# Performance work log

Hardware: AMD Instinct MI355X
Metric: run time of the kernel (lower is better)

Reference implementation:

```python
import jax, jax.numpy as jnp
import numpy as np

B, T, D, H = 1, 2048, 1024, 16
Dh = D // H
GSA_SCALE = 0.25
LN_EPS = 1e-5


def setup_inputs() -> dict:
    key = jax.random.key(0)
    ks = jax.random.split(key, 24)
    s = 0.02
    def W(k, din, dout):
        return jax.random.normal(k, (din, dout), jnp.float32) * s
    inp = dict(
        x=jax.random.normal(ks[0], (B, T, D), jnp.float32),
        mask=jnp.ones((B, T, T), jnp.bool_),
        # MultiHeadAttention params (linears[0..3] = q,k,v,o)
        mha_wq=W(ks[1], D, D), mha_bq=jnp.zeros((D,), jnp.float32),
        mha_wk=W(ks[2], D, D), mha_bk=jnp.zeros((D,), jnp.float32),
        mha_wv=W(ks[3], D, D), mha_bv=jnp.zeros((D,), jnp.float32),
        mha_wo=W(ks[4], D, D), mha_bo=jnp.zeros((D,), jnp.float32),
        # _GeodesicSelfAttention params
        gsa_wq=W(ks[5], D, D), gsa_bq=jnp.zeros((D,), jnp.float32),
        gsa_wk=W(ks[6], D, D), gsa_bk=jnp.zeros((D,), jnp.float32),
        gsa_wv=W(ks[7], D, D), gsa_bv=jnp.zeros((D,), jnp.float32),
        gsa_wo=W(ks[8], D, D), gsa_bo=jnp.zeros((D,), jnp.float32),
        log_diag=jnp.zeros((H, Dh), jnp.float32),  # nn.Parameter(torch.zeros(h, dk))
        # LayerNorms
        ln_mha_g=jnp.ones((D,), jnp.float32), ln_mha_b=jnp.zeros((D,), jnp.float32),
        ln_gsa_g=jnp.ones((D,), jnp.float32), ln_gsa_b=jnp.zeros((D,), jnp.float32),
        # mix scalar (initialized to -2.0 in __init__)
        gsa_mix=jnp.asarray(-2.0, jnp.float32),
        # gate: Linear(D,D) -> GELU -> Linear(D,1), last bias filled with 0.5
        gate_w1=W(ks[9], D, D), gate_b1=jnp.zeros((D,), jnp.float32),
        gate_w2=W(ks[10], D, 1), gate_b2=jnp.full((1,), 0.5, jnp.float32),
    )
    return inp


def _ln(x, g, b):
    m = x.mean(-1, keepdims=True)
    v = ((x - m) ** 2).mean(-1, keepdims=True)
    return (x - m) / jnp.sqrt(v + LN_EPS) * g + b


def _heads(y):  # [B,T,D] -> [B,H,T,Dh]
    return y.reshape(B, T, H, Dh).transpose(0, 2, 1, 3)


def _merge(y):  # [B,H,T,Dh] -> [B,T,D]
    return y.transpose(0, 2, 1, 3).reshape(B, T, D)


def _forward(x, mask, mha_wq, mha_bq, mha_wk, mha_bk, mha_wv, mha_bv, mha_wo, mha_bo,
             gsa_wq, gsa_bq, gsa_wk, gsa_bk, gsa_wv, gsa_bv, gsa_wo, gsa_bo,
             log_diag, ln_mha_g, ln_mha_b, ln_gsa_g, ln_gsa_b, gsa_mix,
             gate_w1, gate_b1, gate_w2, gate_b2):
    inv_sqrt_dh = 1.0 / jnp.sqrt(jnp.float32(Dh))
    m4 = mask[:, None, :, :]  # [B,1,T,T]

    # ---- standard MHA branch ----
    q = _heads(x @ mha_wq + mha_bq)
    k = _heads(x @ mha_wk + mha_bk)
    v = _heads(x @ mha_wv + mha_bv)
    scores = jnp.einsum('bhtd,bhsd->bhts', q, k) * inv_sqrt_dh
    scores = jnp.where(m4, scores, -jnp.inf)
    p = jax.nn.softmax(scores, axis=-1)
    mha_out = _merge(jnp.einsum('bhts,bhsd->bhtd', p, v)) @ mha_wo + mha_bo

    # ---- geodesic (Mahalanobis) branch ----
    qg = _heads(x @ gsa_wq + gsa_bq)
    kg = _heads(x @ gsa_wk + gsa_bk)
    vg = _heads(x @ gsa_wv + gsa_bv)
    diag = jax.nn.softplus(log_diag) + 1e-6          # [H,Dh]
    diag4 = diag[None, :, None, :]
    qM = qg * diag4
    q2M = (qg * qM).sum(-1)                           # [B,H,T]
    k2M = (kg * (kg * diag4)).sum(-1)                 # [B,H,T]
    cross = jnp.einsum('bhtd,bhsd->bhts', qM, kg)     # [B,H,T,T]
    dist = q2M[..., :, None] + k2M[..., None, :] - 2.0 * cross
    s = -0.5 * dist * inv_sqrt_dh
    s = jnp.where(m4, s, -jnp.inf)
    all_inf = jnp.all(jnp.isneginf(s), axis=-1, keepdims=True)
    s = jnp.where(all_inf, 0.0, s)
    pg = jax.nn.softmax(s * GSA_SCALE, axis=-1)
    gsa_out = _merge(jnp.einsum('bhts,bhsd->bhtd', pg, vg)) @ gsa_wo + gsa_bo

    # ---- gated mix ----
    mha_out = _ln(mha_out, ln_mha_g, ln_mha_b)
    gsa_out = jax.nn.sigmoid(gsa_mix) * _ln(gsa_out, ln_gsa_g, ln_gsa_b)
    g = jax.nn.gelu(x @ gate_w1 + gate_b1, approximate=False) @ gate_w2 + gate_b2
    alpha = 0.9 * jax.nn.sigmoid(g)                   # alpha_cap = 0.9, [B,T,1]
    return alpha * mha_out + (1.0 - alpha) * gsa_out


def reference(x, mask, mha_wq, mha_bq, mha_wk, mha_bk, mha_wv, mha_bv, mha_wo, mha_bo,
              gsa_wq, gsa_bq, gsa_wk, gsa_bk, gsa_wv, gsa_bv, gsa_wo, gsa_bo,
              log_diag, ln_mha_g, ln_mha_b, ln_gsa_g, ln_gsa_b, gsa_mix,
              gate_w1, gate_b1, gate_w2, gate_b2):
    return _forward(x, mask, mha_wq, mha_bq, mha_wk, mha_bk, mha_wv, mha_bv, mha_wo, mha_bo,
                    gsa_wq, gsa_bq, gsa_wk, gsa_bk, gsa_wv, gsa_bv, gsa_wo, gsa_bo,
                    log_diag, ln_mha_g, ln_mha_b, ln_gsa_g, ln_gsa_b, gsa_mix,
                    gate_w1, gate_b1, gate_w2, gate_b2)
```

## Files before the change

### kernel.cpp

```cpp
#include <hip/hip_runtime.h>
#include <stdint.h>

typedef unsigned short u16;
typedef u16   u16x4  __attribute__((ext_vector_type(4)));
typedef u16   u16x8  __attribute__((ext_vector_type(8)));
typedef __bf16 bf16x8 __attribute__((ext_vector_type(8)));
typedef float f32x4  __attribute__((ext_vector_type(4)));

#define SEQ   2048
#define DM    1024
#define NHEAD 16
#define DHEAD 64

#define QM_SCALE 0.180336880f
#define QG_SCALE 0.045084220f
#define K2_SCALE 0.022542110f

static __device__ __forceinline__ u16 f2b(float f) {
  uint32_t u = __float_as_uint(f);
  u += 0x7fffu + ((u >> 16) & 1u);
  return (u16)(u >> 16);
}
static __device__ __forceinline__ float b2f(u16 u) {
  return __uint_as_float(((uint32_t)u) << 16);
}

static __device__ __forceinline__ void gload16(const u16* g, u16* l) {
  __builtin_amdgcn_global_load_lds(
      (const __attribute__((address_space(1))) unsigned int*)g,
      (__attribute__((address_space(3))) unsigned int*)l, 16, 0, 0);
}

struct PrepArgs { const float* w[9]; u16* o[9];
                  const float* x; u16* xb; const float* log_diag; float* diag; };

__global__ __launch_bounds__(256) void prep_kernel(PrepArgs a) {
  const int z = blockIdx.z, tid = threadIdx.x;
  if (z == 9) {
    int b = blockIdx.y * 16 + blockIdx.x;
#pragma unroll
    for (int j = 0; j < 8; ++j) {
      int idx = b * 8192 + j * 1024 + tid * 4;
      float4 v = *(const float4*)&a.x[idx];
      u16x4 w = {f2b(v.x), f2b(v.y), f2b(v.z), f2b(v.w)};
      *(u16x4*)&a.xb[idx] = w;
    }
    if (b == 0) {
#pragma unroll
      for (int j = 0; j < 4; ++j) {
        int i = j * 256 + tid;
        float v = a.log_diag[i];
        float sp = (v > 20.f) ? v : log1pf(__expf(v));
        a.diag[i] = sp + 1e-6f;
      }
    }
    return;
  }
  const float* __restrict__ src = a.w[z];
  u16* __restrict__ dst = a.o[z];
  int r0 = blockIdx.y * 64, c0 = blockIdx.x * 64;
  __shared__ float tile[64][65];
  int r = tid >> 2, o8 = (tid & 3) * 16;
#pragma unroll
  for (int i = 0; i < 16; i += 4) {
    float4 v = *(const float4*)&src[(r0 + r) * DM + c0 + o8 + i];
    tile[r][o8 + i + 0] = v.x; tile[r][o8 + i + 1] = v.y;
    tile[r][o8 + i + 2] = v.z; tile[r][o8 + i + 3] = v.w;
  }
  __syncthreads();
  u16x8 w0, w1;
#pragma unroll
  for (int i = 0; i < 8; ++i) w0[i] = f2b(tile[o8 + i][r]);
#pragma unroll
  for (int i = 0; i < 8; ++i) w1[i] = f2b(tile[o8 + 8 + i][r]);
  *(u16x8*)&dst[(c0 + r) * DM + r0 + o8]     = w0;
  *(u16x8*)&dst[(c0 + r) * DM + r0 + o8 + 8] = w1;
}

struct GemmDesc { const u16* A; const u16* Bt; const float* bias; void* out;
                  float* aux; int mode; int k0; int klen; float scale; };
struct GemmParams { GemmDesc d[8]; const float* diag; };

#define MFMA16 __builtin_amdgcn_mfma_f32_16x16x32_bf16

__global__
__attribute__((amdgpu_flat_work_group_size(512, 512)))
__attribute__((amdgpu_waves_per_eu(2, 2)))
void gemm_bt_kernel(GemmParams p) {
  GemmDesc g = p.d[blockIdx.z];
  const int K = DM;
  const int m0 = blockIdx.y * 256, n0 = blockIdx.x * 256;
  const int tid = threadIdx.x;
  const int wave = tid >> 6, lane = tid & 63, ln = lane & 15, quad = lane >> 4;
  const int wm = wave >> 2, wn = wave & 3;

  __shared__ __align__(16) u16 As[2][256 * 64];
  __shared__ __align__(16) u16 Bs[2][256 * 64];

  const f32x4 fz = {0.f, 0.f, 0.f, 0.f};
  f32x4 c00=fz,c01=fz,c02=fz,c03=fz, c10=fz,c11=fz,c12=fz,c13=fz;
  f32x4 c20=fz,c21=fz,c22=fz,c23=fz, c30=fz,c31=fz,c32=fz,c33=fz;
  f32x4 c40=fz,c41=fz,c42=fz,c43=fz, c50=fz,c51=fz,c52=fz,c53=fz;
  f32x4 c60=fz,c61=fz,c62=fz,c63=fz, c70=fz,c71=fz,c72=fz,c73=fz;

  const int trow  = tid >> 3;
  const int dslot = (tid & 7) ^ (trow & 7);
  const u16* Ap = g.A  + (size_t)(m0 + trow) * K + g.k0 + dslot * 8;
  const u16* Bp = g.Bt + (size_t)(n0 + trow) * K + g.k0 + dslot * 8;

  const int swA = (quad ^ (ln & 7)) * 8;
  const int swB = ((4 + quad) ^ (ln & 7)) * 8;
  const int bA = (wm * 128 + ln) * 64;
  const int bB = (wn * 64 + ln) * 64;

#pragma unroll
  for (int s = 0; s < 4; ++s)
    gload16(Ap + (size_t)s * 64 * K, &As[0][s * 4096 + tid * 8]);
#pragma unroll
  for (int s = 0; s < 4; ++s)
    gload16(Bp + (size_t)s * 64 * K, &Bs[0][s * 4096 + tid * 8]);

#define MB_STEP(SW, MB, A0, A1, A2, A3) {                                   \
    bf16x8 af = *(const bf16x8*)&As[cur][bA + (MB)*1024 + (SW)];            \
    A0 = MFMA16(af, b0, A0, 0, 0, 0); A1 = MFMA16(af, b1, A1, 0, 0, 0);     \
    A2 = MFMA16(af, b2, A2, 0, 0, 0); A3 = MFMA16(af, b3, A3, 0, 0, 0); }

#define KH_STEP(SW) {                                                       \
    bf16x8 b0 = *(const bf16x8*)&Bs[cur][bB +    0 + (SW)];                 \
    bf16x8 b1 = *(const bf16x8*)&Bs[cur][bB + 1024 + (SW)];                 \
    bf16x8 b2 = *(const bf16x8*)&Bs[cur][bB + 2048 + (SW)];                 \
    bf16x8 b3 = *(const bf16x8*)&Bs[cur][bB + 3072 + (SW)];                 \
    MB_STEP(SW, 0, c00, c01, c02, c03)  MB_STEP(SW, 1, c10, c11, c12, c13)  \
    MB_STEP(SW, 2, c20, c21, c22, c23)  MB_STEP(SW, 3, c30, c31, c32, c33)  \
    MB_STEP(SW, 4, c40, c41, c42, c43)  MB_STEP(SW, 5, c50, c51, c52, c53)  \
    MB_STEP(SW, 6, c60, c61, c62, c63)  MB_STEP(SW, 7, c70, c71, c72, c73) }

  const int nt = g.klen >> 6;
  int cur = 0;
  for (int t = 0; t < nt; ++t) {
    if (t + 1 < nt) {
      const int kk = (t + 1) << 6;
#pragma unroll
      for (int s = 0; s < 4; ++s)
        gload16(Ap + (size_t)s * 64 * K + kk, &As[cur ^ 1][s * 4096 + tid * 8]);
#pragma unroll
      for (int s = 0; s < 4; ++s)
        gload16(Bp + (size_t)s * 64 * K + kk, &Bs[cur ^ 1][s * 4096 + tid * 8]);
      asm volatile("s_waitcnt vmcnt(8)\n\ts_barrier" ::: "memory");
    } else {
      asm volatile("s_waitcnt vmcnt(0)\n\ts_barrier" ::: "memory");
    }
    KH_STEP(swA)
    KH_STEP(swB)
    asm volatile("s_barrier" ::: "memory");
    cur ^= 1;
  }

  const int mode = g.mode;

#define EPI_ONE(NB, A) {                                                    \
    const int col = n0 + wn * 64 + (NB) * 16 + ln;                          \
    const float bv = g.bias ? g.bias[col] : 0.f;                            \
    if (mode == 5) {                                                        \
      u16x4 w;                                                              \
      _Pragma("unroll") for (int r = 0; r < 4; ++r) w[r] = f2b(A[r] + bv);  \
      *(u16x4*)&((u16*)g.out)[(size_t)col * SEQ + row] = w;                 \
    } else {                                                                \
      _Pragma("unroll") for (int r = 0; r < 4; ++r) {                       \
        float v = A[r] + bv; int rw = row + r;                              \
        if (mode == 0) {                                                    \
          ((u16*)g.out)[((size_t)(col >> 6) * SEQ + rw) * DHEAD + (col & 63)] = f2b(v); \
        } else if (mode == 1) {                                             \
          ((u16*)g.out)[((size_t)(col >> 6) * SEQ + rw) * DHEAD + (col & 63)] = f2b(v * g.scale); \
        } else if (mode == 2) {                                             \
          ((u16*)g.out)[((size_t)(col >> 6) * SEQ + rw) * DHEAD + (col & 63)] = f2b(v * p.diag[col] * g.scale); \
        } else if (mode == 3) {                                             \
          float gg = 0.5f * v * (1.f + erff(v * 0.70710678f));              \
          ((u16*)g.out)[(size_t)rw * DM + col] = f2b(gg);                   \
        } else if (mode == 4) {                                             \
          ((float*)g.out)[(size_t)rw * DM + col] = v;                       \
        } else {                                                            \
          ((u16*)g.out)[((size_t)(col >> 6) * SEQ + rw) * DHEAD + (col & 63)] = f2b(v); \
          ksum[r] += v * v * p.diag[col];                                   \
        }                                                                   \
      }                                                                     \
    } }

#define EPI_ROW(MB, A0, A1, A2, A3) {                                       \
    const int row = m0 + wm * 128 + (MB) * 16 + quad * 4;                   \
    float ksum[4] = {0.f, 0.f, 0.f, 0.f};                                   \
    EPI_ONE(0, A0) EPI_ONE(1, A1) EPI_ONE(2, A2) EPI_ONE(3, A3)             \
    if (mode == 6) {                                                        \
      const int h = (n0 >> 6) + wn;                                         \
      _Pragma("unroll") for (int r = 0; r < 4; ++r) {                       \
        float s = ksum[r];                                                  \
        s += __shfl_xor(s, 1); s += __shfl_xor(s, 2);                       \
        s += __shfl_xor(s, 4); s += __shfl_xor(s, 8);                       \
        if (ln == 0) g.aux[(size_t)h * SEQ + row + r] = s * K2_SCALE;       \
      }                                                                     \
    } }

  EPI_ROW(0, c00, c01, c02, c03)
  EPI_ROW(1, c10, c11, c12, c13)
  EPI_ROW(2, c20, c21, c22, c23)
  EPI_ROW(3, c30, c31, c32, c33)
  EPI_ROW(4, c40, c41, c42, c43)
  EPI_ROW(5, c50, c51, c52, c53)
  EPI_ROW(6, c60, c61, c62, c63)
  EPI_ROW(7, c70, c71, c72, c73)
}

struct ProjArgs { const u16* A[4]; const u16* Bt[4]; const float* bias[4];
                  float* out[4]; int k0[4]; };

__global__ __launch_bounds__(256) void gemm_proj_kernel(ProjArgs pa) {
  const int z = blockIdx.z;
  const u16* __restrict__ A  = pa.A[z];
  const u16* __restrict__ Bt = pa.Bt[z];
  const float* __restrict__ bias = pa.bias[z];
  float* __restrict__ out = pa.out[z];
  const int K = DM, k0 = pa.k0[z];
  const int m0 = blockIdx.y * 128, n0 = blockIdx.x * 128;
  const int tid = threadIdx.x;
  const int wave = tid >> 6, lane = tid & 63, ln = lane & 15, quad = lane >> 4;
  const int wm = wave >> 1, wn = wave & 1;

  __shared__ __align__(16) u16 As[2][128 * 64];
  __shared__ __align__(16) u16 Bs[2][128 * 64];

  const f32x4 fz = {0.f, 0.f, 0.f, 0.f};
  f32x4 d00=fz,d01=fz,d02=fz,d03=fz, d10=fz,d11=fz,d12=fz,d13=fz;
  f32x4 d20=fz,d21=fz,d22=fz,d23=fz, d30=fz,d31=fz,d32=fz,d33=fz;

  const int trow  = tid >> 3;
  const int dslot = (tid & 7) ^ (trow & 7);
  const u16* Ap = A  + (size_t)(m0 + trow) * K + k0 + dslot * 8;
  const u16* Bp = Bt + (size_t)(n0 + trow) * K + k0 + dslot * 8;

  const int swA = (quad ^ (ln & 7)) * 8;
  const int swB = ((4 + quad) ^ (ln & 7)) * 8;
  const int bA = (wm * 64 + ln) * 64;
  const int bB = (wn * 64 + ln) * 64;

#pragma unroll
  for (int s = 0; s < 4; ++s) {
    gload16(Ap + (size_t)s * 32 * K, &As[0][s * 2048 + tid * 8]);
    gload16(Bp + (size_t)s * 32 * K, &Bs[0][s * 2048 + tid * 8]);
  }
  __syncthreads();

#define PMB(SW, MB, D0, D1, D2, D3) {                                       \
    bf16x8 af = *(const bf16x8*)&As[cur][bA + (MB)*1024 + (SW)];            \
    D0 = MFMA16(af, b0, D0, 0, 0, 0); D1 = MFMA16(af, b1, D1, 0, 0, 0);     \
    D2 = MFMA16(af, b2, D2, 0, 0, 0); D3 = MFMA16(af, b3, D3, 0, 0, 0); }

#define PKH(SW) {                                                           \
    bf16x8 b0 = *(const bf16x8*)&Bs[cur][bB +    0 + (SW)];                 \
    bf16x8 b1 = *(const bf16x8*)&Bs[cur][bB + 1024 + (SW)];                 \
    bf16x8 b2 = *(const bf16x8*)&Bs[cur][bB + 2048 + (SW)];                 \
    bf16x8 b3 = *(const bf16x8*)&Bs[cur][bB + 3072 + (SW)];                 \
    PMB(SW, 0, d00, d01, d02, d03)  PMB(SW, 1, d10, d11, d12, d13)          \
    PMB(SW, 2, d20, d21, d22, d23)  PMB(SW, 3, d30, d31, d32, d33) }

  const int nt = 512 >> 6;
  int cur = 0;
  for (int t = 0; t < nt; ++t) {
    if (t + 1 < nt) {
      const int kk = (t + 1) << 6;
#pragma unroll
      for (int s = 0; s < 4; ++s) {
        gload16(Ap + (size_t)s * 32 * K + kk, &As[cur ^ 1][s * 2048 + tid * 8]);
        gload16(Bp + (size_t)s * 32 * K + kk, &Bs[cur ^ 1][s * 2048 + tid * 8]);
      }
    }
    PKH(swA)
    PKH(swB)
    __syncthreads();
    cur ^= 1;
  }

#define EPJ1(NB, D) {                                                       \
    const int col = n0 + wn * 64 + (NB) * 16 + ln;                          \
    const float bv = bias ? bias[col] : 0.f;                                \
    _Pragma("unroll") for (int r = 0; r < 4; ++r)                           \
      out[(size_t)(row + r) * DM + col] = D[r] + bv; }

#define EPJ(MB, D0, D1, D2, D3) {                                           \
    const int row = m0 + wm * 64 + (MB) * 16 + quad * 4;                    \
    EPJ1(0, D0) EPJ1(1, D1) EPJ1(2, D2) EPJ1(3, D3) }

  EPJ(0, d00, d01, d02, d03)
  EPJ(1, d10, d11, d12, d13)
  EPJ(2, d20, d21, d22, d23)
  EPJ(3, d30, d31, d32, d33)
}

__global__ __launch_bounds__(256) void flash_kernel(
    const u16* __restrict__ Qm, const u16* __restrict__ Km, const u16* __restrict__ VmT,
    const u16* __restrict__ Qg, const u16* __restrict__ Kg, const u16* __restrict__ VgT,
    const float* __restrict__ k2m, u16* __restrict__ attM, u16* __restrict__ attG) {
  const int z = blockIdx.z;
  const u16* __restrict__ Q  = z ? Qg  : Qm;
  const u16* __restrict__ Kp = z ? Kg  : Km;
  const u16* __restrict__ Vt = z ? VgT : VmT;
  u16* __restrict__ out = z ? attG : attM;
  const int h = blockIdx.y;
  const int tid = threadIdx.x, wave = tid >> 6, lane = tid & 63, ln = lane & 15, quad = lane >> 4;
  const int wrow = blockIdx.x * 128 + wave * 32;

  __shared__ __align__(16) u16 Ks[64 * 72];
  __shared__ __align__(16) u16 Vs[80 * 72];
  __shared__ __align__(16) u16 Pt[4][32 * 72];
  __shared__ float k2s[64];

  bf16x8 qf[2][2];
#pragma unroll
  for (int qb = 0; qb < 2; ++qb)
#pragma unroll
    for (int kb = 0; kb < 2; ++kb)
      qf[qb][kb] = *(const bf16x8*)&Q[((size_t)(h * SEQ) + wrow + qb * 16 + ln) * 64 + kb * 32 + quad * 8];

  const f32x4 fz = {0.f, 0.f, 0.f, 0.f};
  f32x4 o[2][5];
#pragma unroll
  for (int qb = 0; qb < 2; ++qb)
#pragma unroll
    for (int db = 0; db < 5; ++db) o[qb][db] = fz;

  const int sr = tid >> 2, sc = (tid & 3) * 16;
  const u16* Kbase = Kp + (size_t)h * SEQ * 64;
  const u16* Vbase = Vt + (size_t)h * 64 * SEQ;

  if (tid < 36) ((uint32_t*)&Vs[64 * 72])[tid] = 0x3F803F80u;

  u16x8 kr0 = *(const u16x8*)&Kbase[(size_t)sr * 64 + sc];
  u16x8 kr1 = *(const u16x8*)&Kbase[(size_t)sr * 64 + sc + 8];
  u16x8 vr0 = *(const u16x8*)&Vbase[(size_t)sr * SEQ + sc];
  u16x8 vr1 = *(const u16x8*)&Vbase[(size_t)sr * SEQ + sc + 8];
  float k2r = 0.f;
  if (z && tid < 64) k2r = k2m[h * SEQ + tid];

  for (int kt = 0; kt < SEQ; kt += 64) {
    *(u16x8*)&Ks[sr * 72 + sc]     = kr0;
    *(u16x8*)&Ks[sr * 72 + sc + 8] = kr1;
    *(u16x8*)&Vs[sr * 72 + sc]     = vr0;
    *(u16x8*)&Vs[sr * 72 + sc + 8] = vr1;
    if (z && tid < 64) k2s[tid] = k2r;
    __syncthreads();
    if (kt + 64 < SEQ) {
      kr0 = *(const u16x8*)&Kbase[(size_t)(kt + 64 + sr) * 64 + sc];
      kr1 = *(const u16x8*)&Kbase[(size_t)(kt + 64 + sr) * 64 + sc + 8];
      vr0 = *(const u16x8*)&Vbase[(size_t)sr * SEQ + kt + 64 + sc];
      vr1 = *(const u16x8*)&Vbase[(size_t)sr * SEQ + kt + 64 + sc + 8];
      if (z && tid < 64) k2r = k2m[h * SEQ + kt + 64 + tid];
    }

    bf16x8 kf0[4], kf1[4];
#pragma unroll
    for (int sb = 0; sb < 4; ++sb) {
      kf0[sb] = *(const bf16x8*)&Ks[(sb * 16 + ln) * 72 + quad * 8];
      kf1[sb] = *(const bf16x8*)&Ks[(sb * 16 + ln) * 72 + 32 + quad * 8];
    }

#pragma unroll
    for (int qb = 0; qb < 2; ++qb) {
      f32x4 st[4];
#pragma unroll
      for (int sb = 0; sb < 4; ++sb) {
        st[sb] = fz;
        st[sb] = __builtin_amdgcn_mfma_f32_16x16x32_bf16(kf0[sb], qf[qb][0], st[sb], 0, 0, 0);
        st[sb] = __builtin_amdgcn_mfma_f32_16x16x32_bf16(kf1[sb], qf[qb][1], st[sb], 0, 0, 0);
      }
#pragma unroll
      for (int sb = 0; sb < 4; ++sb) {
        if (z) {
          f32x4 b4 = *(const f32x4*)&k2s[sb * 16 + quad * 4];
#pragma unroll
          for (int r = 0; r < 4; ++r) st[sb][r] -= b4[r];
        }
        uint32_t eb[4];
#pragma unroll
        for (int r = 0; r < 4; ++r)
          eb[r] = __float_as_uint(__builtin_amdgcn_exp2f(st[sb][r]));
        uint32_t lo = __builtin_amdgcn_perm(eb[1], eb[0], 0x07060302u);
        uint32_t hi = __builtin_amdgcn_perm(eb[3], eb[2], 0x07060302u);
        uint2 pk = {lo, hi};
        *(uint2*)&Pt[wave][(qb * 16 + ln) * 72 + sb * 16 + quad * 4] = pk;
      }
    }
    __asm__ __volatile__("" ::: "memory");

    bf16x8 pf[2][2];
#pragma unroll
    for (int qb = 0; qb < 2; ++qb) {
      pf[qb][0] = *(const bf16x8*)&Pt[wave][(qb * 16 + ln) * 72 + quad * 8];
      pf[qb][1] = *(const bf16x8*)&Pt[wave][(qb * 16 + ln) * 72 + 32 + quad * 8];
    }
#pragma unroll
    for (int db = 0; db < 5; ++db) {
      bf16x8 vf0 = *(const bf16x8*)&Vs[(db * 16 + ln) * 72 + quad * 8];
      bf16x8 vf1 = *(const bf16x8*)&Vs[(db * 16 + ln) * 72 + 32 + quad * 8];
#pragma unroll
      for (int qb = 0; qb < 2; ++qb) {
        o[qb][db] = __builtin_amdgcn_mfma_f32_16x16x32_bf16(vf0, pf[qb][0], o[qb][db], 0, 0, 0);
        o[qb][db] = __builtin_amdgcn_mfma_f32_16x16x32_bf16(vf1, pf[qb][1], o[qb][db], 0, 0, 0);
      }
    }
    __syncthreads();
  }

#pragma unroll
  for (int qb = 0; qb < 2; ++qb) {
    float l_all = __shfl(o[qb][4][0], ln);
    float inv = 1.f / l_all;
#pragma unroll
    for (int db = 0; db < 4; ++db) {
      u16x4 w;
#pragma unroll
      for (int r = 0; r < 4; ++r) w[r] = f2b(o[qb][db][r] * inv);
      *(u16x4*)&out[(size_t)(wrow + qb * 16 + ln) * DM + h * 64 + db * 16 + quad * 4] = w;
    }
  }
}

__global__ __launch_bounds__(256) void final_kernel(
    const float* __restrict__ p0, const float* __restrict__ p1,
    const float* __restrict__ p2, const float* __restrict__ p3,
    const u16* __restrict__ G1, const float* __restrict__ w2,
    const float* __restrict__ b2, const float* __restrict__ mixp,
    const float* __restrict__ gm, const float* __restrict__ bm,
    const float* __restrict__ gg, const float* __restrict__ bg,
    float* __restrict__ out) {
  int t = blockIdx.x, tid = threadIdx.x;
  float xm[4], xg[4];
  float sm = 0.f, sm2 = 0.f, sg = 0.f, sg2 = 0.f, sd = 0.f;
#pragma unroll
  for (int j0 = 0; j0 < 4; ++j0) {
    int j = tid + j0 * 256;
    size_t idx = (size_t)t * DM + j;
    float a = p0[idx] + p1[idx];
    float b = p2[idx] + p3[idx];
    xm[j0] = a; xg[j0] = b;
    sm += a; sm2 += a * a; sg += b; sg2 += b * b;
    sd += b2f(G1[idx]) * w2[j];
  }
#pragma unroll
  for (int d = 32; d >= 1; d >>= 1) {
    sm += __shfl_xor(sm, d); sm2 += __shfl_xor(sm2, d);
    sg += __shfl_xor(sg, d); sg2 += __shfl_xor(sg2, d);
    sd += __shfl_xor(sd, d);
  }
  __shared__ float red[5][4];
  int wave = tid >> 6;
  if ((tid & 63) == 0) {
    red[0][wave] = sm; red[1][wave] = sm2; red[2][wave] = sg;
    red[3][wave] = sg2; red[4][wave] = sd;
  }
  __syncthreads();
  sm  = red[0][0] + red[0][1] + red[0][2] + red[0][3];
  sm2 = red[1][0] + red[1][1] + red[1][2] + red[1][3];
  sg  = red[2][0] + red[2][1] + red[2][2] + red[2][3];
  sg2 = red[3][0] + red[3][1] + red[3][2] + red[3][3];
  sd  = red[4][0] + red[4][1] + red[4][2] + red[4][3];

  float mm = sm / DM, vm = fmaxf(sm2 / DM - mm * mm, 0.f);
  float rm = rsqrtf(vm + 1e-5f);
  float mg = sg / DM, vg = fmaxf(sg2 / DM - mg * mg, 0.f);
  float rg = rsqrtf(vg + 1e-5f);
  float alpha = 0.9f / (1.f + __expf(-(sd + b2[0])));
  float mix = 1.f / (1.f + __expf(-mixp[0]));
#pragma unroll
  for (int j0 = 0; j0 < 4; ++j0) {
    int j = tid + j0 * 256;
    float lm = (xm[j0] - mm) * rm * gm[j] + bm[j];
    float lg = (xg[j0] - mg) * rg * gg[j] + bg[j];
    out[(size_t)t * DM + j] = alpha * lm + (1.f - alpha) * mix * lg;
  }
}

extern "C" void kernel_launch(void* const* d_in, const int* in_sizes, int n_in,
                              void* d_out, int out_size, void* d_ws, size_t ws_size,
                              hipStream_t stream) {
  const float* x        = (const float*)d_in[0];
  const float* mha_wq = (const float*)d_in[2];
  const float* mha_bq = (const float*)d_in[3];
  const float* mha_wk = (const float*)d_in[4];
  const float* mha_bk = (const float*)d_in[5];
  const float* mha_wv = (const float*)d_in[6];
  const float* mha_bv = (const float*)d_in[7];
  const float* mha_wo = (const float*)d_in[8];
  const float* mha_bo = (const float*)d_in[9];
  const float* gsa_wq = (const float*)d_in[10];
  const float* gsa_bq = (const float*)d_in[11];
  const float* gsa_wk = (const float*)d_in[12];
  const float* gsa_bk = (const float*)d_in[13];
  const float* gsa_wv = (const float*)d_in[14];
  const float* gsa_bv = (const float*)d_in[15];
  const float* gsa_wo = (const float*)d_in[16];
  const float* gsa_bo = (const float*)d_in[17];
  const float* log_diag = (const float*)d_in[18];
  const float* ln_mha_g = (const float*)d_in[19];
  const float* ln_mha_b = (const float*)d_in[20];
  const float* ln_gsa_g = (const float*)d_in[21];
  const float* ln_gsa_b = (const float*)d_in[22];
  const float* gsa_mix  = (const float*)d_in[23];
  const float* gate_w1  = (const float*)d_in[24];
  const float* gate_b1  = (const float*)d_in[25];
  const float* gate_w2  = (const float*)d_in[26];
  const float* gate_b2  = (const float*)d_in[27];

  char* ws = (char*)d_ws;
  size_t off = 0;
  auto alloc = [&](size_t bytes) -> void* {
    void* p = ws + off;
    off += (bytes + 255) & ~(size_t)255;
    return p;
  };

  u16* xb = (u16*)alloc((size_t)SEQ * DM * 2);
  u16* wT[9];
  for (int i = 0; i < 9; ++i) wT[i] = (u16*)alloc((size_t)DM * DM * 2);
  float* diag = (float*)alloc((size_t)DM * 4);
  u16* Qm  = (u16*)alloc((size_t)SEQ * DM * 2);
  u16* Km  = (u16*)alloc((size_t)SEQ * DM * 2);
  u16* Qg  = (u16*)alloc((size_t)SEQ * DM * 2);
  u16* Kg  = (u16*)alloc((size_t)SEQ * DM * 2);
  u16* VmT = (u16*)alloc((size_t)SEQ * DM * 2);
  u16* VgT = (u16*)alloc((size_t)SEQ * DM * 2);
  float* k2m = (float*)alloc((size_t)NHEAD * SEQ * 4);
  u16* G1   = (u16*)alloc((size_t)SEQ * DM * 2);
  u16* attM = (u16*)alloc((size_t)SEQ * DM * 2);
  u16* attG = (u16*)alloc((size_t)SEQ * DM * 2);
  float* proj3 = (float*)alloc((size_t)SEQ * DM * 4);
  float* proj0 = (float*)Qm;
  float* proj1 = (float*)Qg;
  float* proj2 = (float*)VmT;

  PrepArgs pa;
  pa.w[0] = mha_wq; pa.w[1] = mha_wk; pa.w[2] = mha_wv; pa.w[3] = mha_wo;
  pa.w[4] = gsa_wq; pa.w[5] = gsa_wk; pa.w[6] = gsa_wv; pa.w[7] = gsa_wo;
  pa.w[8] = gate_w1;
  for (int i = 0; i < 9; ++i) pa.o[i] = wT[i];
  pa.x = x; pa.xb = xb; pa.log_diag = log_diag; pa.diag = diag;
  prep_kernel<<<dim3(16, 16, 10), 256, 0, stream>>>(pa);

  GemmParams gp{};
  gp.diag = diag;
  gp.d[0] = {xb, wT[0], mha_bq, (void*)Qm,  nullptr, 1, 0, DM, QM_SCALE};
  gp.d[1] = {xb, wT[1], mha_bk, (void*)Km,  nullptr, 0, 0, DM, 1.f};
  gp.d[2] = {xb, wT[2], mha_bv, (void*)VmT, nullptr, 5, 0, DM, 1.f};
  gp.d[3] = {xb, wT[4], gsa_bq, (void*)Qg,  nullptr, 2, 0, DM, QG_SCALE};
  gp.d[4] = {xb, wT[5], gsa_bk, (void*)Kg,  k2m,     6, 0, DM, 1.f};
  gp.d[5] = {xb, wT[6], gsa_bv, (void*)VgT, nullptr, 5, 0, DM, 1.f};
  gp.d[6] = {xb, wT[8], gate_b1,(void*)G1,  nullptr, 3, 0, DM, 1.f};
  gemm_bt_kernel<<<dim3(4, 8, 7), 512, 0, stream>>>(gp);

  flash_kernel<<<dim3(SEQ / 128, NHEAD, 2), 256, 0, stream>>>(Qm, Km, VmT, Qg, Kg, VgT, k2m, attM, attG);

  ProjArgs pj;
  pj.A[0] = attM; pj.A[1] = attM; pj.A[2] = attG; pj.A[3] = attG;
  pj.Bt[0] = wT[3]; pj.Bt[1] = wT[3]; pj.Bt[2] = wT[7]; pj.Bt[3] = wT[7];
  pj.bias[0] = mha_bo; pj.bias[1] = nullptr; pj.bias[2] = gsa_bo; pj.bias[3] = nullptr;
  pj.out[0] = proj0; pj.out[1] = proj1; pj.out[2] = proj2; pj.out[3] = proj3;
  pj.k0[0] = 0; pj.k0[1] = 512; pj.k0[2] = 0; pj.k0[3] = 512;
  gemm_proj_kernel<<<dim3(8, 16, 4), 256, 0, stream>>>(pj);

  final_kernel<<<SEQ, 256, 0, stream>>>(proj0, proj1, proj2, proj3, G1,
                                        gate_w2, gate_b2, gsa_mix,
                                        ln_mha_g, ln_mha_b, ln_gsa_g, ln_gsa_b,
                                        (float*)d_out);
}
```

Before: 308.9 us.

## Split GEMM K-tile into half-tiles with interleaved prefetch and setprio phases

```diff
diff --git a/kernel.cpp b/kernel.cpp
--- a/kernel.cpp
+++ b/kernel.cpp
@@ -94,8 +94,8 @@
   const int wave = tid >> 6, lane = tid & 63, ln = lane & 15, quad = lane >> 4;
   const int wm = wave >> 2, wn = wave & 3;
 
-  __shared__ __align__(16) u16 As[2][256 * 64];
-  __shared__ __align__(16) u16 Bs[2][256 * 64];
+  __shared__ __align__(16) u16 As[2][16384];
+  __shared__ __align__(16) u16 Bs[2][16384];
 
   const f32x4 fz = {0.f, 0.f, 0.f, 0.f};
   f32x4 c00=fz,c01=fz,c02=fz,c03=fz, c10=fz,c11=fz,c12=fz,c13=fz;
@@ -103,57 +103,121 @@
   f32x4 c40=fz,c41=fz,c42=fz,c43=fz, c50=fz,c51=fz,c52=fz,c53=fz;
   f32x4 c60=fz,c61=fz,c62=fz,c63=fz, c70=fz,c71=fz,c72=fz,c73=fz;
 
-  const int trow  = tid >> 3;
-  const int dslot = (tid & 7) ^ (trow & 7);
-  const u16* Ap = g.A  + (size_t)(m0 + trow) * K + g.k0 + dslot * 8;
-  const u16* Bp = g.Bt + (size_t)(n0 + trow) * K + g.k0 + dslot * 8;
-
-  const int swA = (quad ^ (ln & 7)) * 8;
-  const int swB = ((4 + quad) ^ (ln & 7)) * 8;
-  const int bA = (wm * 128 + ln) * 64;
-  const int bB = (wn * 64 + ln) * 64;
-
-#pragma unroll
-  for (int s = 0; s < 4; ++s)
-    gload16(Ap + (size_t)s * 64 * K, &As[0][s * 4096 + tid * 8]);
-#pragma unroll
-  for (int s = 0; s < 4; ++s)
-    gload16(Bp + (size_t)s * 64 * K, &Bs[0][s * 4096 + tid * 8]);
-
-#define MB_STEP(SW, MB, A0, A1, A2, A3) {                                   \
-    bf16x8 af = *(const bf16x8*)&As[cur][bA + (MB)*1024 + (SW)];            \
-    A0 = MFMA16(af, b0, A0, 0, 0, 0); A1 = MFMA16(af, b1, A1, 0, 0, 0);     \
-    A2 = MFMA16(af, b2, A2, 0, 0, 0); A3 = MFMA16(af, b3, A3, 0, 0, 0); }
-
-#define KH_STEP(SW) {                                                       \
-    bf16x8 b0 = *(const bf16x8*)&Bs[cur][bB +    0 + (SW)];                 \
-    bf16x8 b1 = *(const bf16x8*)&Bs[cur][bB + 1024 + (SW)];                 \
-    bf16x8 b2 = *(const bf16x8*)&Bs[cur][bB + 2048 + (SW)];                 \
-    bf16x8 b3 = *(const bf16x8*)&Bs[cur][bB + 3072 + (SW)];                 \
-    MB_STEP(SW, 0, c00, c01, c02, c03)  MB_STEP(SW, 1, c10, c11, c12, c13)  \
-    MB_STEP(SW, 2, c20, c21, c22, c23)  MB_STEP(SW, 3, c30, c31, c32, c33)  \
-    MB_STEP(SW, 4, c40, c41, c42, c43)  MB_STEP(SW, 5, c50, c51, c52, c53)  \
-    MB_STEP(SW, 6, c60, c61, c62, c63)  MB_STEP(SW, 7, c70, c71, c72, c73) }
+  const int srow   = tid >> 2;
+  const int schunk = (tid & 3) ^ (srow & 3);
+  const u16* ApS = g.A  + (size_t)(m0 + srow) * K + g.k0 + schunk * 8;
+  const u16* BpS = g.Bt + (size_t)(n0 + srow) * K + g.k0 + schunk * 8;
+
+  const int swR = (quad ^ (ln & 3)) * 8;
+  const int bA2 = (wm * 128 + ln) * 32;
+  const int bB2 = (wn * 64 + ln) * 32;
+
+  gload16(ApS,                    &As[0][tid * 8]);
+  gload16(ApS + 128 * K,          &As[0][4096 + tid * 8]);
+  gload16(BpS,                    &Bs[0][tid * 8]);
+  gload16(BpS + 128 * K,          &Bs[0][4096 + tid * 8]);
+  gload16(ApS + 32,               &As[0][8192 + tid * 8]);
+  gload16(ApS + 32 + 128 * K,     &As[0][8192 + 4096 + tid * 8]);
+  gload16(BpS + 32,               &Bs[0][8192 + tid * 8]);
+  gload16(BpS + 32 + 128 * K,     &Bs[0][8192 + 4096 + tid * 8]);
+  asm volatile("s_waitcnt vmcnt(4)" ::: "memory");
+  __builtin_amdgcn_s_barrier();
+
+#define ROW4(AF, B0, B1, B2, B3, C0, C1, C2, C3)                            \
+  C0 = MFMA16(AF, B0, C0, 0, 0, 0);  C1 = MFMA16(AF, B1, C1, 0, 0, 0);      \
+  C2 = MFMA16(AF, B2, C2, 0, 0, 0);  C3 = MFMA16(AF, B3, C3, 0, 0, 0);
 
   const int nt = g.klen >> 6;
-  int cur = 0;
   for (int t = 0; t < nt; ++t) {
-    if (t + 1 < nt) {
-      const int kk = (t + 1) << 6;
-#pragma unroll
-      for (int s = 0; s < 4; ++s)
-        gload16(Ap + (size_t)s * 64 * K + kk, &As[cur ^ 1][s * 4096 + tid * 8]);
-#pragma unroll
-      for (int s = 0; s < 4; ++s)
-        gload16(Bp + (size_t)s * 64 * K + kk, &Bs[cur ^ 1][s * 4096 + tid * 8]);
-      asm volatile("s_waitcnt vmcnt(8)\n\ts_barrier" ::: "memory");
-    } else {
-      asm volatile("s_waitcnt vmcnt(0)\n\ts_barrier" ::: "memory");
-    }
-    KH_STEP(swA)
-    KH_STEP(swB)
-    asm volatile("s_barrier" ::: "memory");
-    cur ^= 1;
+    const int cur = t & 1, nxt = cur ^ 1;
+    const bool pf = (t + 1 < nt);
+    const int kk1 = (t + 1) << 6;
+    bf16x8 b0, b1, b2, b3;
+
+    b0 = *(const bf16x8*)&Bs[cur][bB2 +    0 + swR];
+    b1 = *(const bf16x8*)&Bs[cur][bB2 +  512 + swR];
+    b2 = *(const bf16x8*)&Bs[cur][bB2 + 1024 + swR];
+    b3 = *(const bf16x8*)&Bs[cur][bB2 + 1536 + swR];
+    {
+      bf16x8 a0 = *(const bf16x8*)&As[cur][bA2 +    0 + swR];
+      bf16x8 a1 = *(const bf16x8*)&As[cur][bA2 +  512 + swR];
+      bf16x8 a2 = *(const bf16x8*)&As[cur][bA2 + 1024 + swR];
+      bf16x8 a3 = *(const bf16x8*)&As[cur][bA2 + 1536 + swR];
+      if (pf) {
+        gload16(ApS + kk1,           &As[nxt][tid * 8]);
+        gload16(ApS + 128 * K + kk1, &As[nxt][4096 + tid * 8]);
+      }
+      __builtin_amdgcn_s_barrier();
+      __builtin_amdgcn_s_setprio(1);
+      ROW4(a0, b0, b1, b2, b3, c00, c01, c02, c03)
+      ROW4(a1, b0, b1, b2, b3, c10, c11, c12, c13)
+      ROW4(a2, b0, b1, b2, b3, c20, c21, c22, c23)
+      ROW4(a3, b0, b1, b2, b3, c30, c31, c32, c33)
+      __builtin_amdgcn_s_setprio(0);
+      __builtin_amdgcn_s_barrier();
+    }
+    {
+      bf16x8 a4 = *(const bf16x8*)&As[cur][bA2 + 2048 + swR];
+      bf16x8 a5 = *(const bf16x8*)&As[cur][bA2 + 2560 + swR];
+      bf16x8 a6 = *(const bf16x8*)&As[cur][bA2 + 3072 + swR];
+      bf16x8 a7 = *(const bf16x8*)&As[cur][bA2 + 3584 + swR];
+      if (pf) {
+        gload16(BpS + kk1,           &Bs[nxt][tid * 8]);
+        gload16(BpS + 128 * K + kk1, &Bs[nxt][4096 + tid * 8]);
+        asm volatile("s_waitcnt vmcnt(4)" ::: "memory");
+      } else {
+        asm volatile("s_waitcnt vmcnt(0)" ::: "memory");
+      }
+      __builtin_amdgcn_s_barrier();
+      __builtin_amdgcn_s_setprio(1);
+      ROW4(a4, b0, b1, b2, b3, c40, c41, c42, c43)
+      ROW4(a5, b0, b1, b2, b3, c50, c51, c52, c53)
+      ROW4(a6, b0, b1, b2, b3, c60, c61, c62, c63)
+      ROW4(a7, b0, b1, b2, b3, c70, c71, c72, c73)
+      __builtin_amdgcn_s_setprio(0);
+      __builtin_amdgcn_s_barrier();
+    }
+    b0 = *(const bf16x8*)&Bs[cur][8192 + bB2 +    0 + swR];
+    b1 = *(const bf16x8*)&Bs[cur][8192 + bB2 +  512 + swR];
+    b2 = *(const bf16x8*)&Bs[cur][8192 + bB2 + 1024 + swR];
+    b3 = *(const bf16x8*)&Bs[cur][8192 + bB2 + 1536 + swR];
+    {
+      bf16x8 a0 = *(const bf16x8*)&As[cur][8192 + bA2 +    0 + swR];
+      bf16x8 a1 = *(const bf16x8*)&As[cur][8192 + bA2 +  512 + swR];
+      bf16x8 a2 = *(const bf16x8*)&As[cur][8192 + bA2 + 1024 + swR];
+      bf16x8 a3 = *(const bf16x8*)&As[cur][8192 + bA2 + 1536 + swR];
+      if (pf) {
+        gload16(ApS + 32 + kk1,           &As[nxt][8192 + tid * 8]);
+        gload16(ApS + 32 + 128 * K + kk1, &As[nxt][8192 + 4096 + tid * 8]);
+      }
+      __builtin_amdgcn_s_barrier();
+      __builtin_amdgcn_s_setprio(1);
+      ROW4(a0, b0, b1, b2, b3, c00, c01, c02, c03)
+      ROW4(a1, b0, b1, b2, b3, c10, c11, c12, c13)
+      ROW4(a2, b0, b1, b2, b3, c20, c21, c22, c23)
+      ROW4(a3, b0, b1, b2, b3, c30, c31, c32, c33)
+      __builtin_amdgcn_s_setprio(0);
+      __builtin_amdgcn_s_barrier();
+    }
+    {
+      bf16x8 a4 = *(const bf16x8*)&As[cur][8192 + bA2 + 2048 + swR];
+      bf16x8 a5 = *(const bf16x8*)&As[cur][8192 + bA2 + 2560 + swR];
+      bf16x8 a6 = *(const bf16x8*)&As[cur][8192 + bA2 + 3072 + swR];
+      bf16x8 a7 = *(const bf16x8*)&As[cur][8192 + bA2 + 3584 + swR];
+      if (pf) {
+        gload16(BpS + 32 + kk1,           &Bs[nxt][8192 + tid * 8]);
+        gload16(BpS + 32 + 128 * K + kk1, &Bs[nxt][8192 + 4096 + tid * 8]);
+        asm volatile("s_waitcnt vmcnt(4)" ::: "memory");
+      }
+      __builtin_amdgcn_s_barrier();
+      __builtin_amdgcn_s_setprio(1);
+      ROW4(a4, b0, b1, b2, b3, c40, c41, c42, c43)
+      ROW4(a5, b0, b1, b2, b3, c50, c51, c52, c53)
+      ROW4(a6, b0, b1, b2, b3, c60, c61, c62, c63)
+      ROW4(a7, b0, b1, b2, b3, c70, c71, c72, c73)
+      __builtin_amdgcn_s_setprio(0);
+      __builtin_amdgcn_s_barrier();
+    }
   }
 
   const int mode = g.mode;
```

Measured after the change: 388.4 us. +25.7%, slower.
